# Optimization experiments

Hardware: AMD Instinct MI355X
Metric: run time of the kernel (lower is better)

The kernel has to match this reference:

```python
import jax, jax.numpy as jnp
import numpy as np
import math

D_MODEL = 1024
NUM_HEADS = 16
D_K = D_MODEL // NUM_HEADS
MAX_SEQ_LEN = 2048
THETA = 10000.0
BATCH = 2
SEQ = 2048


def _rope_tables():
    inv_freq = THETA ** (-jnp.arange(0, D_K, 2, dtype=jnp.float32) / D_K)  # [d_k/2]
    pos = jnp.arange(MAX_SEQ_LEN, dtype=jnp.float32)                      # [max_seq]
    ang = pos[:, None] * inv_freq[None, :]                                # [max_seq, d_k/2]
    return jnp.cos(ang), jnp.sin(ang)


def _apply_rope(x, token_positions, cos_tab, sin_tab):
    # x: [b, h, s, d_k]; token_positions: [b, s]
    cos = cos_tab[token_positions][:, None, :, :]  # [b,1,s,d_k/2]
    sin = sin_tab[token_positions][:, None, :, :]
    xp = x.reshape(*x.shape[:-1], D_K // 2, 2)     # interleaved pairs
    xe, xo = xp[..., 0], xp[..., 1]
    oe = xe * cos - xo * sin
    oo = xe * sin + xo * cos
    return jnp.stack((oe, oo), axis=-1).reshape(x.shape)


def setup_inputs() -> dict:
    key = jax.random.key(0)
    ks = jax.random.split(key, 5)
    std = math.sqrt(2.0 / (D_MODEL + D_MODEL))
    x = jax.random.normal(ks[0], (BATCH, SEQ, D_MODEL), dtype=jnp.float32)
    wq = jax.random.normal(ks[1], (D_MODEL, D_MODEL), dtype=jnp.float32) * std
    wk = jax.random.normal(ks[2], (D_MODEL, D_MODEL), dtype=jnp.float32) * std
    wv = jax.random.normal(ks[3], (D_MODEL, D_MODEL), dtype=jnp.float32) * std
    wo = jax.random.normal(ks[4], (D_MODEL, D_MODEL), dtype=jnp.float32) * std
    token_positions = jnp.broadcast_to(jnp.arange(SEQ, dtype=jnp.int32), (BATCH, SEQ))
    return {"x": x, "wq": wq, "wk": wk, "wv": wv, "wo": wo,
            "token_positions": token_positions}


def reference(x, wq, wk, wv, wo, token_positions):
    b, s, _ = x.shape
    cos_tab, sin_tab = _rope_tables()

    def proj_heads(w):
        y = jnp.einsum('oi,bsi->bso', w, x)  # Linear: w[d_out,d_in]
        return y.reshape(b, s, NUM_HEADS, D_K).transpose(0, 2, 1, 3)  # [b,h,s,d_k]

    q = proj_heads(wq)
    k = proj_heads(wk)
    v = proj_heads(wv)
    q = _apply_rope(q, token_positions, cos_tab, sin_tab)
    k = _apply_rope(k, token_positions, cos_tab, sin_tab)

    scores = jnp.einsum('bhqd,bhkd->bhqk', q, k) / math.sqrt(D_K)
    causal = jnp.tril(jnp.ones((s, s), dtype=bool))
    scores = jnp.where(causal, scores, -jnp.inf)
    attn = jax.nn.softmax(scores, axis=-1)
    out = jnp.einsum('bhqk,bhkd->bhqd', attn, v)
    out = out.transpose(0, 2, 1, 3).reshape(b, s, D_MODEL)
    return jnp.einsum('oi,bsi->bso', wo, out)
```

## Files before the change

### kernel.cpp

```cpp
#include <hip/hip_runtime.h>
#include <cstdint>
#include <cstddef>

#define NH 16
#define DK 64
#define DM 1024
#define SEQL 2048
#define NB 2
#define NR (NB * SEQL)

typedef short bf16x8 __attribute__((ext_vector_type(8)));
typedef float f32x4 __attribute__((ext_vector_type(4)));

static __device__ __forceinline__ float bf2f(short u) {
  union { unsigned int i; float f; } x;
  x.i = ((unsigned int)(unsigned short)u) << 16;
  return x.f;
}
static __device__ __forceinline__ short f2bf(float f) {
  union { unsigned int i; float f; } x;
  x.f = f;
  unsigned int r = x.i + 0x7fffu + ((x.i >> 16) & 1u);
  return (short)(r >> 16);
}
static __device__ __forceinline__ unsigned cvtpk(float a, float b) {
  unsigned r;
  asm("v_cvt_pk_bf16_f32 %0, %1, %2" : "=v"(r) : "v"(a), "v"(b));
  return r;
}

static __device__ __forceinline__ void store_out(float* p, float v) { *p = v; }
static __device__ __forceinline__ void store_out(short* p, float v) { *p = f2bf(v); }

static __device__ __forceinline__ void gload16(const short* g, short* l) {
  __builtin_amdgcn_global_load_lds((const __attribute__((address_space(1))) void*)g,
                                   (__attribute__((address_space(3))) void*)l, 16, 0, 0);
}

__global__ void cvt_all(const float* __restrict__ x, const float* __restrict__ w0,
                        const float* __restrict__ w1, const float* __restrict__ w2,
                        const float* __restrict__ w3, short* __restrict__ xb,
                        short* __restrict__ o0, short* __restrict__ o1,
                        short* __restrict__ o2, short* __restrict__ o3) {
  int y = blockIdx.y;
  const float* in;
  short* out;
  if (y < 4) { in = x + (size_t)y * DM * DM; out = xb + (size_t)y * DM * DM; }
  else if (y == 4) { in = w0; out = o0; }
  else if (y == 5) { in = w1; out = o1; }
  else if (y == 6) { in = w2; out = o2; }
  else { in = w3; out = o3; }
  int i = (blockIdx.x * blockDim.x + threadIdx.x) * 4;
  float4 v = *reinterpret_cast<const float4*>(in + i);
  short4 o;
  o.x = f2bf(v.x); o.y = f2bf(v.y); o.z = f2bf(v.z); o.w = f2bf(v.w);
  *reinterpret_cast<short4*>(out + i) = o;
}

__global__ void rope_table_kernel(float2* __restrict__ tab) {
  int idx = blockIdx.x * blockDim.x + threadIdx.x;
  int pos = idx >> 5, j = idx & 31;
  float freq = powf(10000.0f, -(float)j / 32.0f);
  float ang = (float)pos * freq;
  tab[idx] = make_float2(cosf(ang), sinf(ang));
}

__global__ void rope_apply_kernel(short* __restrict__ Qb, short* __restrict__ Kb,
                                  const int* __restrict__ pos, const float2* __restrict__ tab) {
  short* buf = blockIdx.y ? Kb : Qb;
  const float scale = blockIdx.y ? 1.0f : 0.1803368801f;
  int gid = blockIdx.x * blockDim.x + threadIdx.x;
  int elem = gid * 8;
  int row = elem >> 10, off = elem & 1023;
  int j0 = (off & 63) >> 1;
  short* ptr = buf + (size_t)row * DM + off;
  bf16x8 v = *reinterpret_cast<bf16x8*>(ptr);
  const float2* tp = &tab[pos[row] * 32 + j0];
  bf16x8 o;
#pragma unroll
  for (int q = 0; q < 4; ++q) {
    float2 cs = tp[q];
    float xe = bf2f(v[2 * q]), xo = bf2f(v[2 * q + 1]);
    o[2 * q] = f2bf((xe * cs.x - xo * cs.y) * scale);
    o[2 * q + 1] = f2bf((xe * cs.y + xo * cs.x) * scale);
  }
  *reinterpret_cast<bf16x8*>(ptr) = o;
}

__global__ __launch_bounds__(256) void vt_transpose_kernel(const short* __restrict__ V,
                                                           short* __restrict__ Vt) {
  __shared__ short tile[64][64];
  const int t = threadIdx.x;
  const int bh = blockIdx.y, b = bh >> 4, h = bh & 15;
  const int st = blockIdx.x * 64;
#pragma unroll
  for (int p = 0; p < 2; ++p) {
    int c = p * 256 + t;
    int srow = c >> 3, ch = c & 7;
    int chs = ch ^ ((srow >> 3) & 7);
    *reinterpret_cast<bf16x8*>(&tile[srow][chs * 8]) =
        *reinterpret_cast<const bf16x8*>(&V[(size_t)(b * SEQL + st + srow) * DM + h * 64 + ch * 8]);
  }
  __syncthreads();
#pragma unroll
  for (int p = 0; p < 2; ++p) {
    int c = p * 256 + t;
    int drow = c >> 3, soff = (c & 7) * 8;
    short o[8];
#pragma unroll
    for (int e = 0; e < 8; ++e) {
      int srow = soff + e;
      int col = (((drow >> 3) ^ ((srow >> 3) & 7)) << 3) + (drow & 7);
      o[e] = tile[srow][col];
    }
    *reinterpret_cast<bf16x8*>(&Vt[(size_t)(bh * DK + drow) * SEQL + st + soff]) =
        *reinterpret_cast<bf16x8*>(o);
  }
}

template <typename OutT>
static __device__ __forceinline__ void gemm_body(const short* __restrict__ A,
                                                 const short* __restrict__ B,
                                                 OutT* __restrict__ C,
                                                 int m0, int n0, int N, int K) {
  __shared__ short As[128][32];
  __shared__ short Bs[128][32];
  const int t = threadIdx.x;
  const int wid = t >> 6, lane = t & 63;
  const int wr = wid >> 1, wc = wid & 1;
  const int lrow = lane & 15, lk = lane >> 4;

  f32x4 acc[4][4];
#pragma unroll
  for (int i = 0; i < 4; ++i)
#pragma unroll
    for (int j = 0; j < 4; ++j) acc[i][j] = (f32x4){0.f, 0.f, 0.f, 0.f};

  for (int k0 = 0; k0 < K; k0 += 32) {
    __syncthreads();
#pragma unroll
    for (int p = 0; p < 2; ++p) {
      int c = p * 256 + t;
      int row = c >> 2, kc = (c & 3) * 8;
      gload16(&A[(size_t)(m0 + row) * K + k0 + kc], &As[0][0] + (size_t)(p * 256 + wid * 64) * 8);
      gload16(&B[(size_t)(n0 + row) * K + k0 + kc], &Bs[0][0] + (size_t)(p * 256 + wid * 64) * 8);
    }
    __syncthreads();
    bf16x8 af[4], bfr[4];
#pragma unroll
    for (int i = 0; i < 4; ++i) {
      af[i] = *reinterpret_cast<const bf16x8*>(&As[wr * 64 + i * 16 + lrow][lk * 8]);
      bfr[i] = *reinterpret_cast<const bf16x8*>(&Bs[wc * 64 + i * 16 + lrow][lk * 8]);
    }
    __builtin_amdgcn_s_setprio(1);
#pragma unroll
    for (int i = 0; i < 4; ++i)
#pragma unroll
      for (int j = 0; j < 4; ++j)
        acc[i][j] = __builtin_amdgcn_mfma_f32_16x16x32_bf16(af[i], bfr[j], acc[i][j], 0, 0, 0);
    __builtin_amdgcn_s_setprio(0);
  }
#pragma unroll
  for (int i = 0; i < 4; ++i)
#pragma unroll
    for (int j = 0; j < 4; ++j) {
      int row = m0 + wr * 64 + i * 16 + lk * 4;
      int col = n0 + wc * 64 + j * 16 + lrow;
#pragma unroll
      for (int r = 0; r < 4; ++r) store_out(&C[(size_t)(row + r) * N + col], acc[i][j][r]);
    }
}

__global__ __launch_bounds__(256) void qkv_gemm_kernel(
    const short* __restrict__ X, const short* __restrict__ Wq, const short* __restrict__ Wk,
    const short* __restrict__ Wv, short* __restrict__ Q, short* __restrict__ K,
    short* __restrict__ V) {
  int nb = blockIdx.x;
  const short* B = (nb < 8) ? Wq : (nb < 16) ? Wk : Wv;
  short* C = (nb < 8) ? Q : (nb < 16) ? K : V;
  gemm_body<short>(X, B, C, blockIdx.y * 128, (nb & 7) * 128, DM, DM);
}

__global__ __launch_bounds__(256) void out_gemm_kernel(const short* __restrict__ A,
                                                       const short* __restrict__ W,
                                                       float* __restrict__ C) {
  gemm_body<float>(A, W, C, blockIdx.y * 128, blockIdx.x * 128, DM, DM);
}

__global__ __launch_bounds__(256) void attn_kernel(const short* __restrict__ Q,
                                                   const short* __restrict__ K,
                                                   const short* __restrict__ Vt,
                                                   short* __restrict__ O) {
  __shared__ short Ks[64][72];
  __shared__ short Vs[64][72];
  __shared__ short Ps[4][16][72];
  const int t = threadIdx.x;
  const int wid = t >> 6, lane = t & 63;
  const int lrow = lane & 15, lk = lane >> 4;
  const int lin = blockIdx.x;
  const int xcd = lin & 7, idx = lin >> 3;
  const int qt = 31 - (idx >> 2);
  const int bh = xcd * 4 + (idx & 3);
  const int b = bh >> 4, h = bh & 15;
  const size_t base = (size_t)b * SEQL * DM + (size_t)h * DK;
  const size_t vbase = (size_t)bh * DK * SEQL;
  const int kr0 = t >> 3, kr1 = 32 + (t >> 3), ko0 = (t & 7) * 8;
  const float THR = 11.5416f;
  const int qmin = qt * 64 + wid * 16;

  bf16x8 aq[2];
#pragma unroll
  for (int c = 0; c < 2; ++c)
    aq[c] = *reinterpret_cast<const bf16x8*>(
        &Q[base + (size_t)(qmin + lrow) * DM + c * 32 + lk * 8]);

  f32x4 oacc[4];
#pragma unroll
  for (int g = 0; g < 4; ++g) oacc[g] = (f32x4){0.f, 0.f, 0.f, 0.f};
  float mrow = -1e30f, lsum = 0.f;

  {
    bf16x8 k0 = *reinterpret_cast<const bf16x8*>(&K[base + (size_t)kr0 * DM + ko0]);
    bf16x8 k1 = *reinterpret_cast<const bf16x8*>(&K[base + (size_t)kr1 * DM + ko0]);
    bf16x8 v0 = *reinterpret_cast<const bf16x8*>(&Vt[vbase + (size_t)kr0 * SEQL + ko0]);
    bf16x8 v1 = *reinterpret_cast<const bf16x8*>(&Vt[vbase + (size_t)kr1 * SEQL + ko0]);
    *reinterpret_cast<bf16x8*>(&Ks[kr0][ko0]) = k0;
    *reinterpret_cast<bf16x8*>(&Ks[kr1][ko0]) = k1;
    *reinterpret_cast<bf16x8*>(&Vs[kr0][ko0]) = v0;
    *reinterpret_cast<bf16x8*>(&Vs[kr1][ko0]) = v1;
  }
  bf16x8 kreg0, kreg1, vreg0, vreg1;
  for (int kt = 0; kt <= qt; ++kt) {
    __syncthreads();
    if (kt < qt) {
      size_t ko = (size_t)(kt + 1) * 64;
      kreg0 = *reinterpret_cast<const bf16x8*>(&K[base + (ko + kr0) * DM + ko0]);
      kreg1 = *reinterpret_cast<const bf16x8*>(&K[base + (ko + kr1) * DM + ko0]);
      vreg0 = *reinterpret_cast<const bf16x8*>(&Vt[vbase + (size_t)kr0 * SEQL + ko + ko0]);
      vreg1 = *reinterpret_cast<const bf16x8*>(&Vt[vbase + (size_t)kr1 * SEQL + ko + ko0]);
    }
    f32x4 st[4];
    __builtin_amdgcn_s_setprio(1);
#pragma unroll
    for (int g = 0; g < 4; ++g) {
      bf16x8 kf0 = *reinterpret_cast<const bf16x8*>(&Ks[g * 16 + lrow][lk * 8]);
      bf16x8 kf1 = *reinterpret_cast<const bf16x8*>(&Ks[g * 16 + lrow][32 + lk * 8]);
      f32x4 z = (f32x4){0.f, 0.f, 0.f, 0.f};
      z = __builtin_amdgcn_mfma_f32_16x16x32_bf16(kf0, aq[0], z, 0, 0, 0);
      st[g] = __builtin_amdgcn_mfma_f32_16x16x32_bf16(kf1, aq[1], z, 0, 0, 0);
    }
    __builtin_amdgcn_s_setprio(0);
    const int qg = qmin + lrow;
    if (kt == qt) {
#pragma unroll
      for (int g = 0; g < 4; ++g)
#pragma unroll
        for (int r = 0; r < 4; ++r)
          if (kt * 64 + g * 16 + lk * 4 + r > qg) st[g][r] = -1e30f;
    }
    float pmax = st[0][0];
#pragma unroll
    for (int g = 0; g < 4; ++g)
#pragma unroll
      for (int r = 0; r < 4; ++r) pmax = fmaxf(pmax, st[g][r]);
    if (!__all(pmax <= mrow + THR)) {
      float mx = pmax;
      mx = fmaxf(mx, __shfl_xor(mx, 16));
      mx = fmaxf(mx, __shfl_xor(mx, 32));
      float mnew = fmaxf(mrow, mx);
      float alpha = exp2f(mrow - mnew);
      lsum *= alpha;
      float alr[4];
#pragma unroll
      for (int r = 0; r < 4; ++r) alr[r] = __shfl(alpha, lk * 4 + r);
#pragma unroll
      for (int g = 0; g < 4; ++g)
#pragma unroll
        for (int r = 0; r < 4; ++r) oacc[g][r] *= alr[r];
      mrow = mnew;
    }
    float p[4][4], psum = 0.f;
#pragma unroll
    for (int g = 0; g < 4; ++g)
#pragma unroll
      for (int r = 0; r < 4; ++r) {
        float e = exp2f(st[g][r] - mrow);
        p[g][r] = e;
        psum += e;
      }
    lsum += psum;
#pragma unroll
    for (int g = 0; g < 4; ++g) {
      uint2 wv = make_uint2(cvtpk(p[g][0], p[g][1]), cvtpk(p[g][2], p[g][3]));
      *reinterpret_cast<uint2*>(&Ps[wid][lrow][g * 16 + lk * 4]) = wv;
    }
    asm volatile("s_waitcnt lgkmcnt(0)" ::: "memory");
    __builtin_amdgcn_sched_barrier(0);
    bf16x8 pa0 = *reinterpret_cast<const bf16x8*>(&Ps[wid][lrow][lk * 8]);
    bf16x8 pa1 = *reinterpret_cast<const bf16x8*>(&Ps[wid][lrow][32 + lk * 8]);
    __builtin_amdgcn_s_setprio(1);
#pragma unroll
    for (int g = 0; g < 4; ++g) {
      bf16x8 vf0 = *reinterpret_cast<const bf16x8*>(&Vs[g * 16 + lrow][lk * 8]);
      bf16x8 vf1 = *reinterpret_cast<const bf16x8*>(&Vs[g * 16 + lrow][32 + lk * 8]);
      oacc[g] = __builtin_amdgcn_mfma_f32_16x16x32_bf16(pa0, vf0, oacc[g], 0, 0, 0);
      oacc[g] = __builtin_amdgcn_mfma_f32_16x16x32_bf16(pa1, vf1, oacc[g], 0, 0, 0);
    }
    __builtin_amdgcn_s_setprio(0);
    __syncthreads();
    if (kt < qt) {
      *reinterpret_cast<bf16x8*>(&Ks[kr0][ko0]) = kreg0;
      *reinterpret_cast<bf16x8*>(&Ks[kr1][ko0]) = kreg1;
      *reinterpret_cast<bf16x8*>(&Vs[kr0][ko0]) = vreg0;
      *reinterpret_cast<bf16x8*>(&Vs[kr1][ko0]) = vreg1;
    }
  }
  lsum += __shfl_xor(lsum, 16);
  lsum += __shfl_xor(lsum, 32);
  float lr[4];
#pragma unroll
  for (int r = 0; r < 4; ++r) lr[r] = 1.0f / __shfl(lsum, lk * 4 + r);
#pragma unroll
  for (int g = 0; g < 4; ++g)
#pragma unroll
    for (int r = 0; r < 4; ++r)
      O[base + (size_t)(qmin + lk * 4 + r) * DM + g * 16 + lrow] = f2bf(oacc[g][r] * lr[r]);
}

extern "C" void kernel_launch(void* const* d_in, const int* in_sizes, int n_in,
                              void* d_out, int out_size, void* d_ws, size_t ws_size,
                              hipStream_t stream) {
  const float* x = (const float*)d_in[0];
  const float* wq = (const float*)d_in[1];
  const float* wk = (const float*)d_in[2];
  const float* wv = (const float*)d_in[3];
  const float* wo = (const float*)d_in[4];
  const int* tpos = (const int*)d_in[5];
  float* out = (float*)d_out;

  char* w = (char*)d_ws;
  short* xb = (short*)w;  w += (size_t)NR * DM * 2;
  short* wqb = (short*)w; w += (size_t)DM * DM * 2;
  short* wkb = (short*)w; w += (size_t)DM * DM * 2;
  short* wvb = (short*)w; w += (size_t)DM * DM * 2;
  short* wob = (short*)w; w += (size_t)DM * DM * 2;
  short* Qb = (short*)w;  w += (size_t)NR * DM * 2;
  short* Kb = (short*)w;  w += (size_t)NR * DM * 2;
  short* Vb = (short*)w;  w += (size_t)NR * DM * 2;
  short* Ob = (short*)w;  w += (size_t)NR * DM * 2;
  float2* tab = (float2*)w;
  short* Vtb = xb;

  cvt_all<<<dim3(DM * DM / 1024, 8), 256, 0, stream>>>(x, wq, wk, wv, wo, xb, wqb, wkb, wvb, wob);
  rope_table_kernel<<<2048 * 32 / 256, 256, 0, stream>>>(tab);
  qkv_gemm_kernel<<<dim3(24, NR / 128), 256, 0, stream>>>(xb, wqb, wkb, wvb, Qb, Kb, Vb);
  rope_apply_kernel<<<dim3(NR * DM / 8 / 256, 2), 256, 0, stream>>>(Qb, Kb, tpos, tab);
  vt_transpose_kernel<<<dim3(SEQL / 64, NB * NH), 256, 0, stream>>>(Vb, Vtb);
  attn_kernel<<<1024, 256, 0, stream>>>(Qb, Kb, Vtb, Ob);
  out_gemm_kernel<<<dim3(DM / 128, NR / 128), 256, 0, stream>>>(Ob, wob, out);
}
```

Measured before the change: 133.9 us.

## Fuse RoPE and V transpose into QKV GEMM epilogue; use 128-query attention tiles

```diff
diff --git a/kernel.cpp b/kernel.cpp
--- a/kernel.cpp
+++ b/kernel.cpp
@@ -28,9 +28,6 @@
   asm("v_cvt_pk_bf16_f32 %0, %1, %2" : "=v"(r) : "v"(a), "v"(b));
   return r;
 }
-
-static __device__ __forceinline__ void store_out(float* p, float v) { *p = v; }
-static __device__ __forceinline__ void store_out(short* p, float v) { *p = f2bf(v); }
 
 static __device__ __forceinline__ void gload16(const short* g, short* l) {
   __builtin_amdgcn_global_load_lds((const __attribute__((address_space(1))) void*)g,
@@ -65,64 +62,10 @@
   tab[idx] = make_float2(cosf(ang), sinf(ang));
 }
 
-__global__ void rope_apply_kernel(short* __restrict__ Qb, short* __restrict__ Kb,
-                                  const int* __restrict__ pos, const float2* __restrict__ tab) {
-  short* buf = blockIdx.y ? Kb : Qb;
-  const float scale = blockIdx.y ? 1.0f : 0.1803368801f;
-  int gid = blockIdx.x * blockDim.x + threadIdx.x;
-  int elem = gid * 8;
-  int row = elem >> 10, off = elem & 1023;
-  int j0 = (off & 63) >> 1;
-  short* ptr = buf + (size_t)row * DM + off;
-  bf16x8 v = *reinterpret_cast<bf16x8*>(ptr);
-  const float2* tp = &tab[pos[row] * 32 + j0];
-  bf16x8 o;
-#pragma unroll
-  for (int q = 0; q < 4; ++q) {
-    float2 cs = tp[q];
-    float xe = bf2f(v[2 * q]), xo = bf2f(v[2 * q + 1]);
-    o[2 * q] = f2bf((xe * cs.x - xo * cs.y) * scale);
-    o[2 * q + 1] = f2bf((xe * cs.y + xo * cs.x) * scale);
-  }
-  *reinterpret_cast<bf16x8*>(ptr) = o;
-}
-
-__global__ __launch_bounds__(256) void vt_transpose_kernel(const short* __restrict__ V,
-                                                           short* __restrict__ Vt) {
-  __shared__ short tile[64][64];
-  const int t = threadIdx.x;
-  const int bh = blockIdx.y, b = bh >> 4, h = bh & 15;
-  const int st = blockIdx.x * 64;
-#pragma unroll
-  for (int p = 0; p < 2; ++p) {
-    int c = p * 256 + t;
-    int srow = c >> 3, ch = c & 7;
-    int chs = ch ^ ((srow >> 3) & 7);
-    *reinterpret_cast<bf16x8*>(&tile[srow][chs * 8]) =
-        *reinterpret_cast<const bf16x8*>(&V[(size_t)(b * SEQL + st + srow) * DM + h * 64 + ch * 8]);
-  }
-  __syncthreads();
-#pragma unroll
-  for (int p = 0; p < 2; ++p) {
-    int c = p * 256 + t;
-    int drow = c >> 3, soff = (c & 7) * 8;
-    short o[8];
-#pragma unroll
-    for (int e = 0; e < 8; ++e) {
-      int srow = soff + e;
-      int col = (((drow >> 3) ^ ((srow >> 3) & 7)) << 3) + (drow & 7);
-      o[e] = tile[srow][col];
-    }
-    *reinterpret_cast<bf16x8*>(&Vt[(size_t)(bh * DK + drow) * SEQL + st + soff]) =
-        *reinterpret_cast<bf16x8*>(o);
-  }
-}
-
-template <typename OutT>
-static __device__ __forceinline__ void gemm_body(const short* __restrict__ A,
+static __device__ __forceinline__ void gemm_core(const short* __restrict__ A,
                                                  const short* __restrict__ B,
-                                                 OutT* __restrict__ C,
-                                                 int m0, int n0, int N, int K) {
+                                                 int m0, int n0, int K,
+                                                 f32x4 (&acc)[4][4]) {
   __shared__ short As[128][32];
   __shared__ short Bs[128][32];
   const int t = threadIdx.x;
@@ -130,7 +73,6 @@
   const int wr = wid >> 1, wc = wid & 1;
   const int lrow = lane & 15, lk = lane >> 4;
 
-  f32x4 acc[4][4];
 #pragma unroll
   for (int i = 0; i < 4; ++i)
 #pragma unroll
@@ -160,6 +102,71 @@
         acc[i][j] = __builtin_amdgcn_mfma_f32_16x16x32_bf16(af[i], bfr[j], acc[i][j], 0, 0, 0);
     __builtin_amdgcn_s_setprio(0);
   }
+}
+
+__global__ __launch_bounds__(256) void qkv_gemm_kernel(
+    const short* __restrict__ X, const short* __restrict__ Wq, const short* __restrict__ Wk,
+    const short* __restrict__ Wv, const int* __restrict__ tpos,
+    const float2* __restrict__ tab, short* __restrict__ Qb, short* __restrict__ Kb,
+    short* __restrict__ Vt) {
+  const int nb = blockIdx.x;
+  const short* Bw = (nb < 8) ? Wq : (nb < 16) ? Wk : Wv;
+  const int m0 = blockIdx.y * 128, n0 = (nb & 7) * 128;
+  f32x4 acc[4][4];
+  gemm_core(X, Bw, m0, n0, DM, acc);
+
+  const int t = threadIdx.x;
+  const int wid = t >> 6, lane = t & 63;
+  const int wr = wid >> 1, wc = wid & 1;
+  const int lrow = lane & 15, lk = lane >> 4;
+
+  if (nb < 16) {
+    short* C = (nb < 8) ? Qb : Kb;
+    const float scale = (nb < 8) ? 0.1803368801f : 1.0f;
+    const float sgn = (lrow & 1) ? 1.0f : -1.0f;
+#pragma unroll
+    for (int i = 0; i < 4; ++i)
+#pragma unroll
+      for (int j = 0; j < 4; ++j) {
+        int row0 = m0 + wr * 64 + i * 16 + lk * 4;
+        int col = n0 + wc * 64 + j * 16 + lrow;
+        int jf = (col & 63) >> 1;
+#pragma unroll
+        for (int r = 0; r < 4; ++r) {
+          int row = row0 + r;
+          float v = acc[i][j][r];
+          float prt = __shfl_xor(v, 1);
+          float2 cs = tab[(size_t)tpos[row] * 32 + jf];
+          C[(size_t)row * DM + col] = f2bf((v * cs.x + sgn * prt * cs.y) * scale);
+        }
+      }
+  } else {
+#pragma unroll
+    for (int i = 0; i < 4; ++i)
+#pragma unroll
+      for (int j = 0; j < 4; ++j) {
+        int row0 = m0 + wr * 64 + i * 16 + lk * 4;
+        int colv = n0 + wc * 64 + j * 16 + lrow;
+        int hh = colv >> 6, d = colv & 63;
+        int bb = row0 >> 11, s0 = row0 & 2047;
+        uint2 u;
+        u.x = cvtpk(acc[i][j][0], acc[i][j][1]);
+        u.y = cvtpk(acc[i][j][2], acc[i][j][3]);
+        *reinterpret_cast<uint2*>(&Vt[((size_t)((bb * NH + hh) * DK + d)) * SEQL + s0]) = u;
+      }
+  }
+}
+
+__global__ __launch_bounds__(256) void out_gemm_kernel(const short* __restrict__ A,
+                                                       const short* __restrict__ W,
+                                                       float* __restrict__ C) {
+  const int m0 = blockIdx.y * 128, n0 = blockIdx.x * 128;
+  f32x4 acc[4][4];
+  gemm_core(A, W, m0, n0, DM, acc);
+  const int t = threadIdx.x;
+  const int wid = t >> 6, lane = t & 63;
+  const int wr = wid >> 1, wc = wid & 1;
+  const int lrow = lane & 15, lk = lane >> 4;
 #pragma unroll
   for (int i = 0; i < 4; ++i)
 #pragma unroll
@@ -167,46 +174,32 @@
       int row = m0 + wr * 64 + i * 16 + lk * 4;
       int col = n0 + wc * 64 + j * 16 + lrow;
 #pragma unroll
-      for (int r = 0; r < 4; ++r) store_out(&C[(size_t)(row + r) * N + col], acc[i][j][r]);
-    }
-}
-
-__global__ __launch_bounds__(256) void qkv_gemm_kernel(
-    const short* __restrict__ X, const short* __restrict__ Wq, const short* __restrict__ Wk,
-    const short* __restrict__ Wv, short* __restrict__ Q, short* __restrict__ K,
-    short* __restrict__ V) {
-  int nb = blockIdx.x;
-  const short* B = (nb < 8) ? Wq : (nb < 16) ? Wk : Wv;
-  short* C = (nb < 8) ? Q : (nb < 16) ? K : V;
-  gemm_body<short>(X, B, C, blockIdx.y * 128, (nb & 7) * 128, DM, DM);
-}
-
-__global__ __launch_bounds__(256) void out_gemm_kernel(const short* __restrict__ A,
-                                                       const short* __restrict__ W,
-                                                       float* __restrict__ C) {
-  gemm_body<float>(A, W, C, blockIdx.y * 128, blockIdx.x * 128, DM, DM);
-}
-
-__global__ __launch_bounds__(256) void attn_kernel(const short* __restrict__ Q,
+      for (int r = 0; r < 4; ++r) C[(size_t)(row + r) * DM + col] = acc[i][j][r];
+    }
+}
+
+__global__ __launch_bounds__(512) void attn_kernel(const short* __restrict__ Q,
                                                    const short* __restrict__ K,
                                                    const short* __restrict__ Vt,
                                                    short* __restrict__ O) {
   __shared__ short Ks[64][72];
   __shared__ short Vs[64][72];
-  __shared__ short Ps[4][16][72];
+  __shared__ short Ps[8][16][72];
   const int t = threadIdx.x;
   const int wid = t >> 6, lane = t & 63;
   const int lrow = lane & 15, lk = lane >> 4;
   const int lin = blockIdx.x;
   const int xcd = lin & 7, idx = lin >> 3;
-  const int qt = 31 - (idx >> 2);
+  const int qt = (idx < 32) ? (15 - (idx >> 2)) : ((idx - 32) >> 2);
   const int bh = xcd * 4 + (idx & 3);
   const int b = bh >> 4, h = bh & 15;
   const size_t base = (size_t)b * SEQL * DM + (size_t)h * DK;
   const size_t vbase = (size_t)bh * DK * SEQL;
-  const int kr0 = t >> 3, kr1 = 32 + (t >> 3), ko0 = (t & 7) * 8;
+  const int kr = t >> 3, ko = (t & 7) * 8;
   const float THR = 11.5416f;
-  const int qmin = qt * 64 + wid * 16;
+  const int ktmax = 2 * qt + 1;
+  const int qmin = qt * 128 + wid * 16;
+  const int dkt = qmin >> 6;
 
   bf16x8 aq[2];
 #pragma unroll
@@ -220,99 +213,93 @@
   float mrow = -1e30f, lsum = 0.f;
 
   {
-    bf16x8 k0 = *reinterpret_cast<const bf16x8*>(&K[base + (size_t)kr0 * DM + ko0]);
-    bf16x8 k1 = *reinterpret_cast<const bf16x8*>(&K[base + (size_t)kr1 * DM + ko0]);
-    bf16x8 v0 = *reinterpret_cast<const bf16x8*>(&Vt[vbase + (size_t)kr0 * SEQL + ko0]);
-    bf16x8 v1 = *reinterpret_cast<const bf16x8*>(&Vt[vbase + (size_t)kr1 * SEQL + ko0]);
-    *reinterpret_cast<bf16x8*>(&Ks[kr0][ko0]) = k0;
-    *reinterpret_cast<bf16x8*>(&Ks[kr1][ko0]) = k1;
-    *reinterpret_cast<bf16x8*>(&Vs[kr0][ko0]) = v0;
-    *reinterpret_cast<bf16x8*>(&Vs[kr1][ko0]) = v1;
+    bf16x8 k0 = *reinterpret_cast<const bf16x8*>(&K[base + (size_t)kr * DM + ko]);
+    bf16x8 v0 = *reinterpret_cast<const bf16x8*>(&Vt[vbase + (size_t)kr * SEQL + ko]);
+    *reinterpret_cast<bf16x8*>(&Ks[kr][ko]) = k0;
+    *reinterpret_cast<bf16x8*>(&Vs[kr][ko]) = v0;
   }
-  bf16x8 kreg0, kreg1, vreg0, vreg1;
-  for (int kt = 0; kt <= qt; ++kt) {
+  bf16x8 kreg, vreg;
+  for (int kt = 0; kt <= ktmax; ++kt) {
     __syncthreads();
-    if (kt < qt) {
-      size_t ko = (size_t)(kt + 1) * 64;
-      kreg0 = *reinterpret_cast<const bf16x8*>(&K[base + (ko + kr0) * DM + ko0]);
-      kreg1 = *reinterpret_cast<const bf16x8*>(&K[base + (ko + kr1) * DM + ko0]);
-      vreg0 = *reinterpret_cast<const bf16x8*>(&Vt[vbase + (size_t)kr0 * SEQL + ko + ko0]);
-      vreg1 = *reinterpret_cast<const bf16x8*>(&Vt[vbase + (size_t)kr1 * SEQL + ko + ko0]);
-    }
-    f32x4 st[4];
-    __builtin_amdgcn_s_setprio(1);
-#pragma unroll
-    for (int g = 0; g < 4; ++g) {
-      bf16x8 kf0 = *reinterpret_cast<const bf16x8*>(&Ks[g * 16 + lrow][lk * 8]);
-      bf16x8 kf1 = *reinterpret_cast<const bf16x8*>(&Ks[g * 16 + lrow][32 + lk * 8]);
-      f32x4 z = (f32x4){0.f, 0.f, 0.f, 0.f};
-      z = __builtin_amdgcn_mfma_f32_16x16x32_bf16(kf0, aq[0], z, 0, 0, 0);
-      st[g] = __builtin_amdgcn_mfma_f32_16x16x32_bf16(kf1, aq[1], z, 0, 0, 0);
-    }
-    __builtin_amdgcn_s_setprio(0);
-    const int qg = qmin + lrow;
-    if (kt == qt) {
+    if (kt < ktmax) {
+      size_t kof = (size_t)(kt + 1) * 64;
+      kreg = *reinterpret_cast<const bf16x8*>(&K[base + (kof + kr) * DM + ko]);
+      vreg = *reinterpret_cast<const bf16x8*>(&Vt[vbase + (size_t)kr * SEQL + kof + ko]);
+    }
+    if (kt <= dkt) {
+      f32x4 st[4];
+      __builtin_amdgcn_s_setprio(1);
+#pragma unroll
+      for (int g = 0; g < 4; ++g) {
+        bf16x8 kf0 = *reinterpret_cast<const bf16x8*>(&Ks[g * 16 + lrow][lk * 8]);
+        bf16x8 kf1 = *reinterpret_cast<const bf16x8*>(&Ks[g * 16 + lrow][32 + lk * 8]);
+        f32x4 z = (f32x4){0.f, 0.f, 0.f, 0.f};
+        z = __builtin_amdgcn_mfma_f32_16x16x32_bf16(kf0, aq[0], z, 0, 0, 0);
+        st[g] = __builtin_amdgcn_mfma_f32_16x16x32_bf16(kf1, aq[1], z, 0, 0, 0);
+      }
+      __builtin_amdgcn_s_setprio(0);
+      const int qg = qmin + lrow;
+      if (kt == dkt) {
+#pragma unroll
+        for (int g = 0; g < 4; ++g)
+#pragma unroll
+          for (int r = 0; r < 4; ++r)
+            if (kt * 64 + g * 16 + lk * 4 + r > qg) st[g][r] = -1e30f;
+      }
+      float pmax = st[0][0];
 #pragma unroll
       for (int g = 0; g < 4; ++g)
 #pragma unroll
-        for (int r = 0; r < 4; ++r)
-          if (kt * 64 + g * 16 + lk * 4 + r > qg) st[g][r] = -1e30f;
-    }
-    float pmax = st[0][0];
-#pragma unroll
-    for (int g = 0; g < 4; ++g)
-#pragma unroll
-      for (int r = 0; r < 4; ++r) pmax = fmaxf(pmax, st[g][r]);
-    if (!__all(pmax <= mrow + THR)) {
-      float mx = pmax;
-      mx = fmaxf(mx, __shfl_xor(mx, 16));
-      mx = fmaxf(mx, __shfl_xor(mx, 32));
-      float mnew = fmaxf(mrow, mx);
-      float alpha = exp2f(mrow - mnew);
-      lsum *= alpha;
-      float alr[4];
-#pragma unroll
-      for (int r = 0; r < 4; ++r) alr[r] = __shfl(alpha, lk * 4 + r);
+        for (int r = 0; r < 4; ++r) pmax = fmaxf(pmax, st[g][r]);
+      if (!__all(pmax <= mrow + THR)) {
+        float mx = pmax;
+        mx = fmaxf(mx, __shfl_xor(mx, 16));
+        mx = fmaxf(mx, __shfl_xor(mx, 32));
+        float mnew = fmaxf(mrow, mx);
+        float alpha = exp2f(mrow - mnew);
+        lsum *= alpha;
+        float alr[4];
+#pragma unroll
+        for (int r = 0; r < 4; ++r) alr[r] = __shfl(alpha, lk * 4 + r);
+#pragma unroll
+        for (int g = 0; g < 4; ++g)
+#pragma unroll
+          for (int r = 0; r < 4; ++r) oacc[g][r] *= alr[r];
+        mrow = mnew;
+      }
+      float psum = 0.f;
 #pragma unroll
       for (int g = 0; g < 4; ++g)
 #pragma unroll
-        for (int r = 0; r < 4; ++r) oacc[g][r] *= alr[r];
-      mrow = mnew;
-    }
-    float p[4][4], psum = 0.f;
-#pragma unroll
-    for (int g = 0; g < 4; ++g)
-#pragma unroll
-      for (int r = 0; r < 4; ++r) {
-        float e = exp2f(st[g][r] - mrow);
-        p[g][r] = e;
-        psum += e;
-      }
-    lsum += psum;
-#pragma unroll
-    for (int g = 0; g < 4; ++g) {
-      uint2 wv = make_uint2(cvtpk(p[g][0], p[g][1]), cvtpk(p[g][2], p[g][3]));
-      *reinterpret_cast<uint2*>(&Ps[wid][lrow][g * 16 + lk * 4]) = wv;
-    }
-    asm volatile("s_waitcnt lgkmcnt(0)" ::: "memory");
-    __builtin_amdgcn_sched_barrier(0);
-    bf16x8 pa0 = *reinterpret_cast<const bf16x8*>(&Ps[wid][lrow][lk * 8]);
-    bf16x8 pa1 = *reinterpret_cast<const bf16x8*>(&Ps[wid][lrow][32 + lk * 8]);
-    __builtin_amdgcn_s_setprio(1);
-#pragma unroll
-    for (int g = 0; g < 4; ++g) {
-      bf16x8 vf0 = *reinterpret_cast<const bf16x8*>(&Vs[g * 16 + lrow][lk * 8]);
-      bf16x8 vf1 = *reinterpret_cast<const bf16x8*>(&Vs[g * 16 + lrow][32 + lk * 8]);
-      oacc[g] = __builtin_amdgcn_mfma_f32_16x16x32_bf16(pa0, vf0, oacc[g], 0, 0, 0);
-      oacc[g] = __builtin_amdgcn_mfma_f32_16x16x32_bf16(pa1, vf1, oacc[g], 0, 0, 0);
-    }
-    __builtin_amdgcn_s_setprio(0);
+        for (int r = 0; r < 4; ++r) {
+          float e = exp2f(st[g][r] - mrow);
+          st[g][r] = e;
+          psum += e;
+        }
+      lsum += psum;
+#pragma unroll
+      for (int g = 0; g < 4; ++g) {
+        uint2 wv = make_uint2(cvtpk(st[g][0], st[g][1]), cvtpk(st[g][2], st[g][3]));
+        *reinterpret_cast<uint2*>(&Ps[wid][lrow][g * 16 + lk * 4]) = wv;
+      }
+      asm volatile("s_waitcnt lgkmcnt(0)" ::: "memory");
+      __builtin_amdgcn_sched_barrier(0);
+      bf16x8 pa0 = *reinterpret_cast<const bf16x8*>(&Ps[wid][lrow][lk * 8]);
+      bf16x8 pa1 = *reinterpret_cast<const bf16x8*>(&Ps[wid][lrow][32 + lk * 8]);
+      __builtin_amdgcn_s_setprio(1);
+#pragma unroll
+      for (int g = 0; g < 4; ++g) {
+        bf16x8 vf0 = *reinterpret_cast<const bf16x8*>(&Vs[g * 16 + lrow][lk * 8]);
+        bf16x8 vf1 = *reinterpret_cast<const bf16x8*>(&Vs[g * 16 + lrow][32 + lk * 8]);
+        oacc[g] = __builtin_amdgcn_mfma_f32_16x16x32_bf16(pa0, vf0, oacc[g], 0, 0, 0);
+        oacc[g] = __builtin_amdgcn_mfma_f32_16x16x32_bf16(pa1, vf1, oacc[g], 0, 0, 0);
+      }
+      __builtin_amdgcn_s_setprio(0);
+    }
     __syncthreads();
-    if (kt < qt) {
-      *reinterpret_cast<bf16x8*>(&Ks[kr0][ko0]) = kreg0;
-      *reinterpret_cast<bf16x8*>(&Ks[kr1][ko0]) = kreg1;
-      *reinterpret_cast<bf16x8*>(&Vs[kr0][ko0]) = vreg0;
-      *reinterpret_cast<bf16x8*>(&Vs[kr1][ko0]) = vreg1;
+    if (kt < ktmax) {
+      *reinterpret_cast<bf16x8*>(&Ks[kr][ko]) = kreg;
+      *reinterpret_cast<bf16x8*>(&Vs[kr][ko]) = vreg;
     }
   }
   lsum += __shfl_xor(lsum, 16);
@@ -346,16 +333,14 @@
   short* wob = (short*)w; w += (size_t)DM * DM * 2;
   short* Qb = (short*)w;  w += (size_t)NR * DM * 2;
   short* Kb = (short*)w;  w += (size_t)NR * DM * 2;
-  short* Vb = (short*)w;  w += (size_t)NR * DM * 2;
+  short* Vtb = (short*)w; w += (size_t)NR * DM * 2;
   short* Ob = (short*)w;  w += (size_t)NR * DM * 2;
   float2* tab = (float2*)w;
-  short* Vtb = xb;
-
+
+  rope_table_kernel<<<2048 * 32 / 256, 256, 0, stream>>>(tab);
   cvt_all<<<dim3(DM * DM / 1024, 8), 256, 0, stream>>>(x, wq, wk, wv, wo, xb, wqb, wkb, wvb, wob);
-  rope_table_kernel<<<2048 * 32 / 256, 256, 0, stream>>>(tab);
-  qkv_gemm_kernel<<<dim3(24, NR / 128), 256, 0, stream>>>(xb, wqb, wkb, wvb, Qb, Kb, Vb);
-  rope_apply_kernel<<<dim3(NR * DM / 8 / 256, 2), 256, 0, stream>>>(Qb, Kb, tpos, tab);
-  vt_transpose_kernel<<<dim3(SEQL / 64, NB * NH), 256, 0, stream>>>(Vb, Vtb);
-  attn_kernel<<<1024, 256, 0, stream>>>(Qb, Kb, Vtb, Ob);
+  qkv_gemm_kernel<<<dim3(24, NR / 128), 256, 0, stream>>>(xb, wqb, wkb, wvb, tpos, tab,
+                                                          Qb, Kb, Vtb);
+  attn_kernel<<<512, 512, 0, stream>>>(Qb, Kb, Vtb, Ob);
   out_gemm_kernel<<<dim3(DM / 128, NR / 128), 256, 0, stream>>>(Ob, wob, out);
 }
```

Result: slower. 138.3 us (+3.3%).
